# Kernel optimization log

Measured on AMD Instinct MI355X. Metric: run time of the kernel, lower is better.

The kernel has to match this reference:

```python
import jax, jax.numpy as jnp
import numpy as np

S = 1.0 / np.sqrt(2.0).astype(np.float32)  # Haar normalization


def _dwt_axis(x, axis):
    """Level-1 Haar DWT along `axis` (length must be even).
    Returns (lo, hi), each half-length along axis."""
    x = jnp.moveaxis(x, axis, -1)
    n = x.shape[-1]
    xp = x.reshape(x.shape[:-1] + (n // 2, 2))
    lo = (xp[..., 0] + xp[..., 1]) * S
    hi = (xp[..., 0] - xp[..., 1]) * S
    return jnp.moveaxis(lo, -1, axis), jnp.moveaxis(hi, -1, axis)


def _idwt_axis(lo, hi, axis, orig_len):
    """Inverse level-1 Haar along `axis`: interleave (lo+hi)*s, (lo-hi)*s."""
    lo = jnp.moveaxis(lo, axis, -1)
    hi = jnp.moveaxis(hi, axis, -1)
    even = (lo + hi) * S
    odd = (lo - hi) * S
    rec = jnp.stack([even, odd], axis=-1).reshape(lo.shape[:-1] + (2 * lo.shape[-1],))
    rec = rec[..., :orig_len]
    return jnp.moveaxis(rec, -1, axis)


def _mix(sub, W, b):
    # 1x1 conv = channel mixing: (B,C,H,W), W: (Cout,Cin), b: (Cout,)
    return jnp.einsum('oc,bchw->bohw', W, sub) + b[None, :, None, None]


def setup_inputs() -> dict:
    key = jax.random.key(0)
    B, C, H, W = 8, 64, 256, 256
    ks = jax.random.split(key, 9)
    scale = 1.0 / C
    inp = {'x': jax.random.normal(ks[0], (B, C, H, W), dtype=jnp.float32)}
    for i, name in enumerate(['LL', 'LH', 'HL', 'HH']):
        inp[f'w_{name}'] = jax.random.uniform(ks[1 + i], (C, C), jnp.float32, -scale, scale)
        inp[f'b_{name}'] = jnp.zeros((C,), jnp.float32)
    return inp


def reference(x, w_LL, b_LL, w_LH, b_LH, w_HL, b_HL, w_HH, b_HH):
    B, C, H, W = x.shape
    # DWT: along W then along H (separable Haar)
    Lw, Hw = _dwt_axis(x, -1)
    LL, LH = _dwt_axis(Lw, -2)
    HL, HH = _dwt_axis(Hw, -2)
    # Per-subband 1x1 channel mixers
    LL = _mix(LL, w_LL, b_LL)
    LH = _mix(LH, w_LH, b_LH)
    HL = _mix(HL, w_HL, b_HL)
    HH = _mix(HH, w_HH, b_HH)
    # IDWT: along H then along W
    Lw_r = _idwt_axis(LL, LH, -2, H)
    Hw_r = _idwt_axis(HL, HH, -2, H)
    return _idwt_axis(Lw_r, Hw_r, -1, W)
```

## Files before the change

### kernel.cpp

```cpp
#include <hip/hip_runtime.h>
#include <hip/hip_bf16.h>


using bf16x8 = __attribute__((ext_vector_type(8))) short;
using f32x4  = __attribute__((ext_vector_type(4))) float;
using f32x2  = __attribute__((ext_vector_type(2))) float;

__device__ inline unsigned short f2bf(float v) {
    __hip_bfloat16 h = __float2bfloat16(v);
    return __builtin_bit_cast(unsigned short, h);
}

__global__ __launch_bounds__(256) void wvc_prep(
    const float* __restrict__ wLL, const float* __restrict__ bLL,
    const float* __restrict__ wLH, const float* __restrict__ bLH,
    const float* __restrict__ wHL, const float* __restrict__ bHL,
    const float* __restrict__ wHH, const float* __restrict__ bHH,
    unsigned short* __restrict__ afrag, float* __restrict__ bcomb)
{
    const int idx  = blockIdx.x * 256 + threadIdx.x;
    const int i    = idx & 7;
    const int lane = (idx >> 3) & 63;
    const int mt   = (idx >> 9) & 3;
    const int ks   = (idx >> 11) & 1;
    const int band = (idx >> 12) & 3;
    const float* Ws[4] = {wLL, wLH, wHL, wHH};
    const int o = mt * 16 + (lane & 15);
    const int c = ks * 32 + (lane >> 4) * 8 + i;
    afrag[idx] = f2bf(0.5f * Ws[band][o * 64 + c]);

    if (blockIdx.x == 0 && threadIdx.x < 64) {
        const int t = threadIdx.x;
        float b0 = bLL[t], b1 = bLH[t], b2 = bHL[t], b3 = bHH[t];
        bcomb[0 * 64 + t] = 0.5f * (b0 + b1 + b2 + b3);
        bcomb[1 * 64 + t] = 0.5f * (b0 + b1 - b2 - b3);
        bcomb[2 * 64 + t] = 0.5f * (b0 - b1 + b2 - b3);
        bcomb[3 * 64 + t] = 0.5f * (b0 - b1 - b2 + b3);
    }
}

#define NT 16
__global__ __launch_bounds__(512, 1) void wvc_main(
    const float* __restrict__ x,
    const unsigned short* __restrict__ afrag_g,
    const float* __restrict__ bcomb,
    float* __restrict__ out)
{
    __shared__ __align__(64) unsigned char lds_x[3][33024];
    __shared__ __align__(16) float lds_bc[256];

    const int tid = threadIdx.x;
    const int l   = tid & 63;
    const int wv  = tid >> 6;
    const int blk = blockIdx.x;
    const int b   = blk >> 5;
    const int jq  = (blk >> 3) & 3;
    const int ih  = blk & 7;
    const int w0  = jq * 64;

    const int sg   = wv & 1;
    const int mt   = wv >> 1;
    const int site = sg * 16 + (l & 15);
    const int lg   = l >> 4;

    if (tid < 256) lds_bc[tid] = bcomb[tid];

    const unsigned short* afb = afrag_g + (size_t)l * 8;
    bf16x8 a[4][2];
    #pragma unroll
    for (int bd = 0; bd < 4; ++bd)
        #pragma unroll
        for (int ks = 0; ks < 2; ++ks)
            a[bd][ks] = *(const bf16x8*)(
                afb + (size_t)((bd * 2 + ks) * 4 + mt) * 512);

    const float* xb = x + (size_t)b * 4194304
                        + (size_t)(wv * 8 + (l >> 5)) * 65536
                        + (size_t)((l >> 4) & 1) * 256 + w0 + (l & 15) * 4;
    const int lbo = wv * 4096 + wv * 32;

    #pragma unroll
    for (int pt = 0; pt < 2; ++pt) {
        const float* g = xb + (size_t)(ih * 16 + pt) * 512;
        unsigned char* lbn = &lds_x[pt][lbo];
        #pragma unroll
        for (int k = 0; k < 4; ++k)
            __builtin_amdgcn_global_load_lds(
                (const __attribute__((address_space(1))) void*)(g + (size_t)(2 * k) * 65536),
                (__attribute__((address_space(3))) void*)(lbn + k * 1024),
                16, 0, 0);
    }
    asm volatile("s_waitcnt lgkmcnt(0)" ::: "memory");

    #pragma unroll
    for (int t = 0; t < NT; ++t) {
        if (t + 2 < NT) {
            const float* g = xb + (size_t)(ih * 16 + t + 2) * 512;
            unsigned char* lbn = &lds_x[(t + 2) % 3][lbo];
            #pragma unroll
            for (int k = 0; k < 4; ++k)
                __builtin_amdgcn_global_load_lds(
                    (const __attribute__((address_space(1))) void*)(g + (size_t)(2 * k) * 65536),
                    (__attribute__((address_space(3))) void*)(lbn + k * 1024),
                    16, 0, 0);
        }
        if (t == 0)            asm volatile("s_waitcnt vmcnt(8)"  ::: "memory");
        else if (t + 2 < NT)   asm volatile("s_waitcnt vmcnt(16)" ::: "memory");
        else if (t + 1 < NT)   asm volatile("s_waitcnt vmcnt(12)" ::: "memory");
        else                   asm volatile("s_waitcnt vmcnt(8)"  ::: "memory");
        __builtin_amdgcn_sched_barrier(0);
        __builtin_amdgcn_s_barrier();
        __builtin_amdgcn_sched_barrier(0);

        const unsigned char* bx = lds_x[t % 3];

        bf16x8 bfr[4][2];
        #pragma unroll
        for (int ks = 0; ks < 2; ++ks) {
            float2 p0[8], p1[8];
            #pragma unroll
            for (int i = 0; i < 8; ++i) {
                const unsigned char* base =
                    bx + (size_t)(ks * 32 + lg * 8 + i) * 512
                       + (ks * 4 + lg) * 32 + site * 8;
                p0[i] = *(const float2*)(base);
                p1[i] = *(const float2*)(base + 256);
            }
            #pragma unroll
            for (int i = 0; i < 8; ++i) {
                float aa = p0[i].x + p0[i].y, mm = p0[i].x - p0[i].y;
                float cc = p1[i].x + p1[i].y, dd = p1[i].x - p1[i].y;
                bfr[0][ks][i] = (short)f2bf(aa + cc);
                bfr[1][ks][i] = (short)f2bf(aa - cc);
                bfr[2][ks][i] = (short)f2bf(mm + dd);
                bfr[3][ks][i] = (short)f2bf(mm - dd);
            }
        }

        f32x4 acc[4];
        #pragma unroll
        for (int bd = 0; bd < 4; ++bd)
            acc[bd] = (f32x4){0.f, 0.f, 0.f, 0.f};
        #pragma unroll
        for (int bd = 0; bd < 4; ++bd)
            #pragma unroll
            for (int ks = 0; ks < 2; ++ks)
                acc[bd] = __builtin_amdgcn_mfma_f32_16x16x32_bf16(
                    a[bd][ks], bfr[bd][ks], acc[bd], 0, 0, 0);

        const int h0 = (ih * 16 + t) * 2;
        float* ob = out + (size_t)b * 4194304 + (size_t)h0 * 256 + w0 + 2 * site;
        const int ob0 = mt * 16 + lg * 4;
        f32x4 bc0 = *(const f32x4*)(&lds_bc[  0 + ob0]);
        f32x4 bc1 = *(const f32x4*)(&lds_bc[ 64 + ob0]);
        f32x4 bc2 = *(const f32x4*)(&lds_bc[128 + ob0]);
        f32x4 bc3 = *(const f32x4*)(&lds_bc[192 + ob0]);
        #pragma unroll
        for (int r = 0; r < 4; ++r) {
            float y0 = acc[0][r];
            float y1 = acc[1][r];
            float y2 = acc[2][r];
            float y3 = acc[3][r];
            float s01 = y0 + y1, d01 = y0 - y1;
            float s23 = y2 + y3, d23 = y2 - y3;
            f32x2 v0; v0[0] = 0.5f * (s01 + s23) + bc0[r];
                      v0[1] = 0.5f * (s01 - s23) + bc1[r];
            f32x2 v1; v1[0] = 0.5f * (d01 + d23) + bc2[r];
                      v1[1] = 0.5f * (d01 - d23) + bc3[r];
            float* po = ob + (size_t)(ob0 + r) * 65536;
            __builtin_nontemporal_store(v0, (f32x2*)po);
            __builtin_nontemporal_store(v1, (f32x2*)(po + 256));
        }

        __builtin_amdgcn_sched_barrier(0);
        __builtin_amdgcn_s_barrier();
        __builtin_amdgcn_sched_barrier(0);
    }
}

extern "C" void kernel_launch(void* const* d_in, const int* in_sizes, int n_in,
                              void* d_out, int out_size, void* d_ws, size_t ws_size,
                              hipStream_t stream) {
    const float* x   = (const float*)d_in[0];
    const float* wLL = (const float*)d_in[1];
    const float* bLL = (const float*)d_in[2];
    const float* wLH = (const float*)d_in[3];
    const float* bLH = (const float*)d_in[4];
    const float* wHL = (const float*)d_in[5];
    const float* bHL = (const float*)d_in[6];
    const float* wHH = (const float*)d_in[7];
    const float* bHH = (const float*)d_in[8];
    float* out = (float*)d_out;

    unsigned short* afrag = (unsigned short*)d_ws;
    float* bcomb = (float*)((char*)d_ws + 32768);

    wvc_prep<<<64, 256, 0, stream>>>(wLL, bLL, wLH, bLH, wHL, bHL, wHH, bHH,
                                     afrag, bcomb);
    wvc_main<<<256, 512, 0, stream>>>(x, afrag, bcomb, out);
}
```

Measured before the change: 52.66 us.

## Retile main kernel to full-width rows with K-split double-buffered stages

Each block now covers full 256-wide rows across 4 row-pairs instead of a 64-wide column quarter. Each stage loads half the input channels, so the K dimension is split across two pipeline stages with a 2-deep LDS ring of larger buffers instead of a 3-deep ring of small ones. Each wave now computes two site groups by two output tiles, reusing weight fragments across more MFMAs. The intent is longer contiguous global loads and better operand reuse, at the cost of more accumulator registers and shallower prefetch.

```diff
diff --git a/kernel.cpp b/kernel.cpp
--- a/kernel.cpp
+++ b/kernel.cpp
@@ -39,14 +39,14 @@
     }
 }
 
-#define NT 16
+#define NT 8
 __global__ __launch_bounds__(512, 1) void wvc_main(
     const float* __restrict__ x,
     const unsigned short* __restrict__ afrag_g,
     const float* __restrict__ bcomb,
     float* __restrict__ out)
 {
-    __shared__ __align__(64) unsigned char lds_x[3][33024];
+    __shared__ __align__(64) unsigned char lds_x[2][65792];
     __shared__ __align__(16) float lds_bc[256];
 
     const int tid = threadIdx.x;
@@ -54,128 +54,144 @@
     const int wv  = tid >> 6;
     const int blk = blockIdx.x;
     const int b   = blk >> 5;
-    const int jq  = (blk >> 3) & 3;
-    const int ih  = blk & 7;
-    const int w0  = jq * 64;
-
-    const int sg   = wv & 1;
-    const int mt   = wv >> 1;
-    const int site = sg * 16 + (l & 15);
-    const int lg   = l >> 4;
+    const int ihg = blk & 31;
+
+    const int sgp   = wv >> 1;
+    const int mth   = wv & 1;
+    const int lg    = l >> 4;
+    const int sbase = sgp * 32 + (l & 15);
 
     if (tid < 256) lds_bc[tid] = bcomb[tid];
 
     const unsigned short* afb = afrag_g + (size_t)l * 8;
-    bf16x8 a[4][2];
+    bf16x8 a[4][2][2];
     #pragma unroll
     for (int bd = 0; bd < 4; ++bd)
         #pragma unroll
-        for (int ks = 0; ks < 2; ++ks)
-            a[bd][ks] = *(const bf16x8*)(
-                afb + (size_t)((bd * 2 + ks) * 4 + mt) * 512);
-
-    const float* xb = x + (size_t)b * 4194304
-                        + (size_t)(wv * 8 + (l >> 5)) * 65536
-                        + (size_t)((l >> 4) & 1) * 256 + w0 + (l & 15) * 4;
-    const int lbo = wv * 4096 + wv * 32;
-
-    #pragma unroll
-    for (int pt = 0; pt < 2; ++pt) {
-        const float* g = xb + (size_t)(ih * 16 + pt) * 512;
-        unsigned char* lbn = &lds_x[pt][lbo];
-        #pragma unroll
-        for (int k = 0; k < 4; ++k)
-            __builtin_amdgcn_global_load_lds(
-                (const __attribute__((address_space(1))) void*)(g + (size_t)(2 * k) * 65536),
-                (__attribute__((address_space(3))) void*)(lbn + k * 1024),
-                16, 0, 0);
+        for (int kh = 0; kh < 2; ++kh)
+            #pragma unroll
+            for (int mtl = 0; mtl < 2; ++mtl)
+                a[bd][kh][mtl] = *(const bf16x8*)(
+                    afb + (size_t)((bd * 2 + kh) * 4 + 2 * mth + mtl) * 512);
+
+    const float* xbase = x + (size_t)b * 4194304 + (size_t)l * 4;
+
+    #define STAGE(s)                                                          \
+    {                                                                         \
+        unsigned char* lb = &lds_x[(s) & 1][0];                               \
+        const int kh_ = (s) & 1;                                              \
+        const int h0_ = 8 * ihg + 2 * ((s) >> 1);                             \
+        _Pragma("unroll")                                                     \
+        for (int k = 0; k < 8; ++k) {                                         \
+            const int chl = wv * 4 + (k >> 1);                                \
+            const float* g = xbase + (size_t)(kh_ * 32 + chl) * 65536         \
+                                   + (size_t)(h0_ + (k & 1)) * 256;           \
+            __builtin_amdgcn_global_load_lds(                                 \
+                (const __attribute__((address_space(1))) void*)g,             \
+                (__attribute__((address_space(3))) void*)(                    \
+                    lb + chl * 2048 + (chl >> 3) * 64 + (k & 1) * 1024        \
+                       + l * 16),                                             \
+                16, 0, 0);                                                    \
+        }                                                                     \
     }
+
+    STAGE(0);
     asm volatile("s_waitcnt lgkmcnt(0)" ::: "memory");
+
+    f32x4 acc[2][2][4];
 
     #pragma unroll
     for (int t = 0; t < NT; ++t) {
-        if (t + 2 < NT) {
-            const float* g = xb + (size_t)(ih * 16 + t + 2) * 512;
-            unsigned char* lbn = &lds_x[(t + 2) % 3][lbo];
-            #pragma unroll
-            for (int k = 0; k < 4; ++k)
-                __builtin_amdgcn_global_load_lds(
-                    (const __attribute__((address_space(1))) void*)(g + (size_t)(2 * k) * 65536),
-                    (__attribute__((address_space(3))) void*)(lbn + k * 1024),
-                    16, 0, 0);
+        const int kh = t & 1;
+        if (t + 1 < NT) STAGE(t + 1);
+        if (t == 0)        asm volatile("s_waitcnt vmcnt(8)"  ::: "memory");
+        else if (kh == 0)  asm volatile("s_waitcnt vmcnt(40)" ::: "memory");
+        else if (t < NT-1) asm volatile("s_waitcnt vmcnt(8)"  ::: "memory");
+        else               asm volatile("s_waitcnt vmcnt(0)"  ::: "memory");
+        __builtin_amdgcn_sched_barrier(0);
+        __builtin_amdgcn_s_barrier();
+        __builtin_amdgcn_sched_barrier(0);
+
+        const unsigned char* bx = lds_x[kh];
+
+        if (kh == 0) {
+            #pragma unroll
+            for (int sgq = 0; sgq < 2; ++sgq)
+                #pragma unroll
+                for (int mtl = 0; mtl < 2; ++mtl)
+                    #pragma unroll
+                    for (int bd = 0; bd < 4; ++bd)
+                        acc[sgq][mtl][bd] = (f32x4){0.f, 0.f, 0.f, 0.f};
         }
-        if (t == 0)            asm volatile("s_waitcnt vmcnt(8)"  ::: "memory");
-        else if (t + 2 < NT)   asm volatile("s_waitcnt vmcnt(16)" ::: "memory");
-        else if (t + 1 < NT)   asm volatile("s_waitcnt vmcnt(12)" ::: "memory");
-        else                   asm volatile("s_waitcnt vmcnt(8)"  ::: "memory");
-        __builtin_amdgcn_sched_barrier(0);
-        __builtin_amdgcn_s_barrier();
-        __builtin_amdgcn_sched_barrier(0);
-
-        const unsigned char* bx = lds_x[t % 3];
-
-        bf16x8 bfr[4][2];
+
         #pragma unroll
-        for (int ks = 0; ks < 2; ++ks) {
+        for (int sgq = 0; sgq < 2; ++sgq) {
+            const int site = sbase + sgq * 16;
             float2 p0[8], p1[8];
             #pragma unroll
             for (int i = 0; i < 8; ++i) {
                 const unsigned char* base =
-                    bx + (size_t)(ks * 32 + lg * 8 + i) * 512
-                       + (ks * 4 + lg) * 32 + site * 8;
+                    bx + (size_t)(lg * 8 + i) * 2048 + lg * 64 + site * 8;
                 p0[i] = *(const float2*)(base);
-                p1[i] = *(const float2*)(base + 256);
+                p1[i] = *(const float2*)(base + 1024);
             }
+            bf16x8 bfr[4];
             #pragma unroll
             for (int i = 0; i < 8; ++i) {
                 float aa = p0[i].x + p0[i].y, mm = p0[i].x - p0[i].y;
                 float cc = p1[i].x + p1[i].y, dd = p1[i].x - p1[i].y;
-                bfr[0][ks][i] = (short)f2bf(aa + cc);
-                bfr[1][ks][i] = (short)f2bf(aa - cc);
-                bfr[2][ks][i] = (short)f2bf(mm + dd);
-                bfr[3][ks][i] = (short)f2bf(mm - dd);
+                bfr[0][i] = (short)f2bf(aa + cc);
+                bfr[1][i] = (short)f2bf(aa - cc);
+                bfr[2][i] = (short)f2bf(mm + dd);
+                bfr[3][i] = (short)f2bf(mm - dd);
+            }
+            #pragma unroll
+            for (int bd = 0; bd < 4; ++bd)
+                #pragma unroll
+                for (int mtl = 0; mtl < 2; ++mtl)
+                    acc[sgq][mtl][bd] = __builtin_amdgcn_mfma_f32_16x16x32_bf16(
+                        a[bd][kh][mtl], bfr[bd], acc[sgq][mtl][bd], 0, 0, 0);
+        }
+
+        if (kh == 1) {
+            const int h0 = 8 * ihg + 2 * (t >> 1);
+            #pragma unroll
+            for (int sgq = 0; sgq < 2; ++sgq) {
+                const int site = sbase + sgq * 16;
+                float* ob = out + (size_t)b * 4194304 + (size_t)h0 * 256
+                                + 2 * site;
+                #pragma unroll
+                for (int mtl = 0; mtl < 2; ++mtl) {
+                    const int ob0 = (2 * mth + mtl) * 16 + lg * 4;
+                    f32x4 bc0 = *(const f32x4*)(&lds_bc[  0 + ob0]);
+                    f32x4 bc1 = *(const f32x4*)(&lds_bc[ 64 + ob0]);
+                    f32x4 bc2 = *(const f32x4*)(&lds_bc[128 + ob0]);
+                    f32x4 bc3 = *(const f32x4*)(&lds_bc[192 + ob0]);
+                    #pragma unroll
+                    for (int r = 0; r < 4; ++r) {
+                        float y0 = acc[sgq][mtl][0][r];
+                        float y1 = acc[sgq][mtl][1][r];
+                        float y2 = acc[sgq][mtl][2][r];
+                        float y3 = acc[sgq][mtl][3][r];
+                        float s01 = y0 + y1, d01 = y0 - y1;
+                        float s23 = y2 + y3, d23 = y2 - y3;
+                        f32x2 v0; v0[0] = 0.5f * (s01 + s23) + bc0[r];
+                                  v0[1] = 0.5f * (s01 - s23) + bc1[r];
+                        f32x2 v1; v1[0] = 0.5f * (d01 + d23) + bc2[r];
+                                  v1[1] = 0.5f * (d01 - d23) + bc3[r];
+                        float* po = ob + (size_t)(ob0 + r) * 65536;
+                        __builtin_nontemporal_store(v0, (f32x2*)po);
+                        __builtin_nontemporal_store(v1, (f32x2*)(po + 256));
+                    }
+                }
             }
         }
 
-        f32x4 acc[4];
-        #pragma unroll
-        for (int bd = 0; bd < 4; ++bd)
-            acc[bd] = (f32x4){0.f, 0.f, 0.f, 0.f};
-        #pragma unroll
-        for (int bd = 0; bd < 4; ++bd)
-            #pragma unroll
-            for (int ks = 0; ks < 2; ++ks)
-                acc[bd] = __builtin_amdgcn_mfma_f32_16x16x32_bf16(
-                    a[bd][ks], bfr[bd][ks], acc[bd], 0, 0, 0);
-
-        const int h0 = (ih * 16 + t) * 2;
-        float* ob = out + (size_t)b * 4194304 + (size_t)h0 * 256 + w0 + 2 * site;
-        const int ob0 = mt * 16 + lg * 4;
-        f32x4 bc0 = *(const f32x4*)(&lds_bc[  0 + ob0]);
-        f32x4 bc1 = *(const f32x4*)(&lds_bc[ 64 + ob0]);
-        f32x4 bc2 = *(const f32x4*)(&lds_bc[128 + ob0]);
-        f32x4 bc3 = *(const f32x4*)(&lds_bc[192 + ob0]);
-        #pragma unroll
-        for (int r = 0; r < 4; ++r) {
-            float y0 = acc[0][r];
-            float y1 = acc[1][r];
-            float y2 = acc[2][r];
-            float y3 = acc[3][r];
-            float s01 = y0 + y1, d01 = y0 - y1;
-            float s23 = y2 + y3, d23 = y2 - y3;
-            f32x2 v0; v0[0] = 0.5f * (s01 + s23) + bc0[r];
-                      v0[1] = 0.5f * (s01 - s23) + bc1[r];
-            f32x2 v1; v1[0] = 0.5f * (d01 + d23) + bc2[r];
-                      v1[1] = 0.5f * (d01 - d23) + bc3[r];
-            float* po = ob + (size_t)(ob0 + r) * 65536;
-            __builtin_nontemporal_store(v0, (f32x2*)po);
-            __builtin_nontemporal_store(v1, (f32x2*)(po + 256));
-        }
-
         __builtin_amdgcn_sched_barrier(0);
         __builtin_amdgcn_s_barrier();
         __builtin_amdgcn_sched_barrier(0);
     }
+    #undef STAGE
 }
 
 extern "C" void kernel_launch(void* const* d_in, const int* in_sizes, int n_in,
```

After: 57.22 us. +8.6%, slower.

## Replace LDS-staged async pipeline with direct per-wave global loads

Applied to the files above, without the earlier changes.

Drops the triple-buffered LDS staging with global_load_lds and block barriers, and has each wave read its input tile straight from global memory into registers. Blocks shrink to 256 threads with two blocks per CU, and the grid doubles. Bias is loaded once into registers instead of through LDS. Each of the four waves now re-reads the same input, which relies on cache hits, and the explicit multi-stage prefetch is lost.

```diff
diff --git a/kernel.cpp b/kernel.cpp
--- a/kernel.cpp
+++ b/kernel.cpp
@@ -40,30 +40,21 @@
 }
 
 #define NT 16
-__global__ __launch_bounds__(512, 1) void wvc_main(
+__global__ __launch_bounds__(256, 2) void wvc_main(
     const float* __restrict__ x,
     const unsigned short* __restrict__ afrag_g,
     const float* __restrict__ bcomb,
     float* __restrict__ out)
 {
-    __shared__ __align__(64) unsigned char lds_x[3][33024];
-    __shared__ __align__(16) float lds_bc[256];
-
     const int tid = threadIdx.x;
     const int l   = tid & 63;
-    const int wv  = tid >> 6;
+    const int mt  = tid >> 6;
     const int blk = blockIdx.x;
-    const int b   = blk >> 5;
-    const int jq  = (blk >> 3) & 3;
-    const int ih  = blk & 7;
-    const int w0  = jq * 64;
-
-    const int sg   = wv & 1;
-    const int mt   = wv >> 1;
-    const int site = sg * 16 + (l & 15);
-    const int lg   = l >> 4;
-
-    if (tid < 256) lds_bc[tid] = bcomb[tid];
+    const int b   = blk >> 6;
+    const int seg = (blk >> 3) & 7;
+    const int hpg = blk & 7;
+    const int lg  = l >> 4;
+    const int site = seg * 16 + (l & 15);
 
     const unsigned short* afb = afrag_g + (size_t)l * 8;
     bf16x8 a[4][2];
@@ -74,68 +65,45 @@
             a[bd][ks] = *(const bf16x8*)(
                 afb + (size_t)((bd * 2 + ks) * 4 + mt) * 512);
 
-    const float* xb = x + (size_t)b * 4194304
-                        + (size_t)(wv * 8 + (l >> 5)) * 65536
-                        + (size_t)((l >> 4) & 1) * 256 + w0 + (l & 15) * 4;
-    const int lbo = wv * 4096 + wv * 32;
+    const int ob0 = mt * 16 + lg * 4;
+    f32x4 bc0 = *(const f32x4*)(bcomb +   0 + ob0);
+    f32x4 bc1 = *(const f32x4*)(bcomb +  64 + ob0);
+    f32x4 bc2 = *(const f32x4*)(bcomb + 128 + ob0);
+    f32x4 bc3 = *(const f32x4*)(bcomb + 192 + ob0);
 
-    #pragma unroll
-    for (int pt = 0; pt < 2; ++pt) {
-        const float* g = xb + (size_t)(ih * 16 + pt) * 512;
-        unsigned char* lbn = &lds_x[pt][lbo];
-        #pragma unroll
-        for (int k = 0; k < 4; ++k)
-            __builtin_amdgcn_global_load_lds(
-                (const __attribute__((address_space(1))) void*)(g + (size_t)(2 * k) * 65536),
-                (__attribute__((address_space(3))) void*)(lbn + k * 1024),
-                16, 0, 0);
-    }
-    asm volatile("s_waitcnt lgkmcnt(0)" ::: "memory");
+    const float* xb = x + (size_t)b * 4194304 + (size_t)(lg * 8) * 65536
+                        + (size_t)(hpg * 16) * 512 + 2 * site;
+    float* obase = out + (size_t)b * 4194304 + (size_t)ob0 * 65536
+                       + (size_t)(hpg * 16) * 512 + 2 * site;
 
     #pragma unroll
     for (int t = 0; t < NT; ++t) {
-        if (t + 2 < NT) {
-            const float* g = xb + (size_t)(ih * 16 + t + 2) * 512;
-            unsigned char* lbn = &lds_x[(t + 2) % 3][lbo];
+        float2 p0[2][8], p1[2][8];
+        #pragma unroll
+        for (int ks = 0; ks < 2; ++ks)
             #pragma unroll
-            for (int k = 0; k < 4; ++k)
-                __builtin_amdgcn_global_load_lds(
-                    (const __attribute__((address_space(1))) void*)(g + (size_t)(2 * k) * 65536),
-                    (__attribute__((address_space(3))) void*)(lbn + k * 1024),
-                    16, 0, 0);
-        }
-        if (t == 0)            asm volatile("s_waitcnt vmcnt(8)"  ::: "memory");
-        else if (t + 2 < NT)   asm volatile("s_waitcnt vmcnt(16)" ::: "memory");
-        else if (t + 1 < NT)   asm volatile("s_waitcnt vmcnt(12)" ::: "memory");
-        else                   asm volatile("s_waitcnt vmcnt(8)"  ::: "memory");
+            for (int i = 0; i < 8; ++i) {
+                const float* pp = xb + (size_t)(ks * 32 + i) * 65536
+                                     + (size_t)t * 512;
+                p0[ks][i] = *(const float2*)pp;
+                p1[ks][i] = *(const float2*)(pp + 256);
+            }
         __builtin_amdgcn_sched_barrier(0);
-        __builtin_amdgcn_s_barrier();
-        __builtin_amdgcn_sched_barrier(0);
-
-        const unsigned char* bx = lds_x[t % 3];
 
         bf16x8 bfr[4][2];
         #pragma unroll
-        for (int ks = 0; ks < 2; ++ks) {
-            float2 p0[8], p1[8];
+        for (int ks = 0; ks < 2; ++ks)
             #pragma unroll
             for (int i = 0; i < 8; ++i) {
-                const unsigned char* base =
-                    bx + (size_t)(ks * 32 + lg * 8 + i) * 512
-                       + (ks * 4 + lg) * 32 + site * 8;
-                p0[i] = *(const float2*)(base);
-                p1[i] = *(const float2*)(base + 256);
-            }
-            #pragma unroll
-            for (int i = 0; i < 8; ++i) {
-                float aa = p0[i].x + p0[i].y, mm = p0[i].x - p0[i].y;
-                float cc = p1[i].x + p1[i].y, dd = p1[i].x - p1[i].y;
+                float aa = p0[ks][i].x + p0[ks][i].y;
+                float mm = p0[ks][i].x - p0[ks][i].y;
+                float cc = p1[ks][i].x + p1[ks][i].y;
+                float dd = p1[ks][i].x - p1[ks][i].y;
                 bfr[0][ks][i] = (short)f2bf(aa + cc);
                 bfr[1][ks][i] = (short)f2bf(aa - cc);
                 bfr[2][ks][i] = (short)f2bf(mm + dd);
                 bfr[3][ks][i] = (short)f2bf(mm - dd);
             }
-        }
 
         f32x4 acc[4];
         #pragma unroll
@@ -148,13 +116,7 @@
                 acc[bd] = __builtin_amdgcn_mfma_f32_16x16x32_bf16(
                     a[bd][ks], bfr[bd][ks], acc[bd], 0, 0, 0);
 
-        const int h0 = (ih * 16 + t) * 2;
-        float* ob = out + (size_t)b * 4194304 + (size_t)h0 * 256 + w0 + 2 * site;
-        const int ob0 = mt * 16 + lg * 4;
-        f32x4 bc0 = *(const f32x4*)(&lds_bc[  0 + ob0]);
-        f32x4 bc1 = *(const f32x4*)(&lds_bc[ 64 + ob0]);
-        f32x4 bc2 = *(const f32x4*)(&lds_bc[128 + ob0]);
-        f32x4 bc3 = *(const f32x4*)(&lds_bc[192 + ob0]);
+        float* ob = obase + (size_t)t * 512;
         #pragma unroll
         for (int r = 0; r < 4; ++r) {
             float y0 = acc[0][r];
@@ -167,13 +129,10 @@
                       v0[1] = 0.5f * (s01 - s23) + bc1[r];
             f32x2 v1; v1[0] = 0.5f * (d01 + d23) + bc2[r];
                       v1[1] = 0.5f * (d01 - d23) + bc3[r];
-            float* po = ob + (size_t)(ob0 + r) * 65536;
+            float* po = ob + (size_t)r * 65536;
             __builtin_nontemporal_store(v0, (f32x2*)po);
             __builtin_nontemporal_store(v1, (f32x2*)(po + 256));
         }
-
-        __builtin_amdgcn_sched_barrier(0);
-        __builtin_amdgcn_s_barrier();
         __builtin_amdgcn_sched_barrier(0);
     }
 }
@@ -197,5 +156,5 @@
 
     wvc_prep<<<64, 256, 0, stream>>>(wLL, bLL, wLH, bLH, wHL, bHL, wHH, bHH,
                                      afrag, bcomb);
-    wvc_main<<<256, 512, 0, stream>>>(x, afrag, bcomb, out);
+    wvc_main<<<512, 256, 0, stream>>>(x, afrag, bcomb, out);
 }
```

Measured after the change: 61.96 us. 17.7% more time.
